# Kernel tuning notes

Hardware: AMD Instinct MI355X
Metric: run time of the kernel (lower is better)

## Reference

```python
import jax, jax.numpy as jnp
import numpy as np

B, S, D, H, INNER = 2, 2048, 1024, 16, 4096
HD = D // H
EPS = 1e-5


def setup_inputs() -> dict:
    key = jax.random.key(0)
    ks = jax.random.split(key, 8)

    def w(k, o, i):
        return jax.random.normal(k, (o, i), jnp.float32) * 0.02

    return {
        "hidden_states": jax.random.normal(ks[0], (B, S, D), jnp.float32),
        "attention_mask": jnp.ones((B, S), jnp.float32),
        "wq": w(ks[1], D, D), "bq": jnp.zeros((D,), jnp.float32),
        "wk": w(ks[2], D, D), "bk": jnp.zeros((D,), jnp.float32),
        "wv": w(ks[3], D, D), "bv": jnp.zeros((D,), jnp.float32),
        "wo": w(ks[4], D, D), "bo": jnp.zeros((D,), jnp.float32),
        "w1": w(ks[5], INNER, D), "b1": jnp.zeros((INNER,), jnp.float32),
        "w2": w(ks[6], D, INNER), "b2": jnp.zeros((D,), jnp.float32),
        "g1": jnp.ones((D,), jnp.float32), "be1": jnp.zeros((D,), jnp.float32),
        "g2": jnp.ones((D,), jnp.float32), "be2": jnp.zeros((D,), jnp.float32),
        "w_bits": 8,
        "a_bits": 8,
    }


def fake_quant(x, bits):
    # symmetric per-tensor fake quantization with straight-through estimator
    qmax = 2.0 ** (bits - 1) - 1.0
    scale = jnp.maximum(jnp.max(jnp.abs(x)), 1e-8) / qmax
    q = jnp.round(jnp.clip(x / scale, -qmax, qmax)) * scale
    return x + jax.lax.stop_gradient(q - x)


def qlinear(x, w, b, w_bits, a_bits):
    return fake_quant(x, a_bits) @ fake_quant(w, w_bits).T + b


def layernorm(x, g, b):
    m = jnp.mean(x, axis=-1, keepdims=True)
    v = jnp.mean((x - m) ** 2, axis=-1, keepdims=True)
    return (x - m) * jax.lax.rsqrt(v + EPS) * g + b


def reference(hidden_states, attention_mask, wq, bq, wk, bk, wv, bv, wo, bo,
              w1, b1, w2, b2, g1, be1, g2, be2, w_bits, a_bits):
    # --- attention sub-block ---
    residual = hidden_states
    x = layernorm(hidden_states, g1, be1)
    q = qlinear(x, wq, bq, w_bits, a_bits).reshape(B, S, H, HD)
    k = qlinear(x, wk, bk, w_bits, a_bits).reshape(B, S, H, HD)
    v = qlinear(x, wv, bv, w_bits, a_bits).reshape(B, S, H, HD)
    scores = jnp.einsum("bqhd,bkhd->bhqk", q, k) / jnp.sqrt(jnp.float32(HD))
    scores = scores + (1.0 - attention_mask)[:, None, None, :] * -10000.0
    probs = jax.nn.softmax(scores, axis=-1)
    attn = jnp.einsum("bhqk,bkhd->bqhd", probs, v).reshape(B, S, D)
    attn = qlinear(attn, wo, bo, w_bits, a_bits)
    hidden = residual + attn
    # --- MLP sub-block ---
    residual = hidden
    x = layernorm(hidden, g2, be2)
    x = qlinear(x, w1, b1, w_bits, a_bits)
    x = jax.nn.gelu(x, approximate=False)
    x = qlinear(x, w2, b2, w_bits, a_bits)
    return residual + x
```

## Files before the change

### kernel.cpp

```cpp
#include <hip/hip_runtime.h>
#include <hip/hip_bf16.h>
#include <math.h>

typedef __bf16 bf16;
typedef __bf16 bf16x8 __attribute__((ext_vector_type(8)));
typedef __bf16 bf16x4 __attribute__((ext_vector_type(4)));
typedef float  f32x4  __attribute__((ext_vector_type(4)));
typedef float  f32x16 __attribute__((ext_vector_type(16)));
typedef unsigned int u32x4 __attribute__((ext_vector_type(4)));

static constexpr int B_  = 2;
static constexpr int S_  = 2048;
static constexpr int D_  = 1024;
static constexpr int H_  = 16;
static constexpr int HD_ = 64;
static constexpr int I_  = 4096;
static constexpr int NT  = B_ * S_;

__device__ __forceinline__ void atomicMaxF(float* p, float v) {
  atomicMax((unsigned int*)p, __float_as_uint(v));
}

__device__ __forceinline__ f32x4 mfma16(bf16x8 a, bf16x8 b, f32x4 c) {
  return __builtin_amdgcn_mfma_f32_16x16x32_bf16(a, b, c, 0, 0, 0);
}

__device__ __forceinline__ f32x16 mfma32(bf16x8 a, bf16x8 b, f32x16 c) {
  return __builtin_amdgcn_mfma_f32_32x32x16_bf16(a, b, c, 0, 0, 0);
}

__device__ __forceinline__ void gload16(const void* g, void* lds) {
  __builtin_amdgcn_global_load_lds(
      (const __attribute__((address_space(1))) void*)g,
      (__attribute__((address_space(3))) void*)lds, 16, 0, 0);
}

__device__ __forceinline__ float quant1(float x, float scale, float qmax) {
  return rintf(fminf(fmaxf(x / scale, -qmax), qmax)) * scale;
}

__device__ __forceinline__ void stage64b(const bf16* __restrict__ g, int rs, bf16* lds, int t) {
  #pragma unroll
  for (int r = 0; r < 4; r++) {
    const int cl  = r * 128 + t;
    const int row = cl >> 3;
    const int scr = (cl & 7) ^ (row & 7);
    gload16(g + (size_t)row * rs + scr * 8,
            (char*)lds + (size_t)(r * 128 + (t & 64)) * 16);
  }
}

__global__ __launch_bounds__(256) void k_prep(const float* __restrict__ mask,
                                              float* __restrict__ madd, float* __restrict__ scal) {
  constexpr float MSK2 = -14426.950408889634f;
  const int i = blockIdx.x * 256 + threadIdx.x;
  if (blockIdx.x == 0 && threadIdx.x < 32) scal[threadIdx.x] = 0.f;
  if (i < B_ * S_) madd[i] = (1.0f - mask[i]) * MSK2;
}

struct WArgs {
  const float* w[6];
  bf16* q[6];
  size_t n4[6];
};

__global__ __launch_bounds__(256) void k_absmax6(WArgs a, float* __restrict__ slots) {
  const int z = blockIdx.z;
  const float* __restrict__ x = a.w[z];
  const size_t n4 = a.n4[z];
  size_t i = (size_t)blockIdx.x * 256 + threadIdx.x;
  const size_t stride = (size_t)gridDim.x * 256;
  float m = 0.f;
  for (; i < n4; i += stride) {
    float4 v = ((const float4*)x)[i];
    m = fmaxf(m, fmaxf(fmaxf(fabsf(v.x), fabsf(v.y)), fmaxf(fabsf(v.z), fabsf(v.w))));
  }
  #pragma unroll
  for (int o = 32; o; o >>= 1) m = fmaxf(m, __shfl_xor(m, o));
  __shared__ float red[4];
  if ((threadIdx.x & 63) == 0) red[threadIdx.x >> 6] = m;
  __syncthreads();
  if (threadIdx.x == 0)
    atomicMaxF(slots + z, fmaxf(fmaxf(red[0], red[1]), fmaxf(red[2], red[3])));
}

__global__ __launch_bounds__(256) void k_quant6(WArgs a, const float* __restrict__ slots,
                                                const int* __restrict__ bits) {
  const int z = blockIdx.z;
  const float* __restrict__ x = a.w[z];
  bf16* __restrict__ y = a.q[z];
  const size_t n4 = a.n4[z];
  const float qmax  = (float)((1 << (*bits - 1)) - 1);
  const float scale = fmaxf(slots[z], 1e-8f) / qmax;
  size_t i = (size_t)blockIdx.x * 256 + threadIdx.x;
  const size_t stride = (size_t)gridDim.x * 256;
  for (; i < n4; i += stride) {
    float4 v = ((const float4*)x)[i];
    bf16x4 o;
    o[0] = (bf16)quant1(v.x, scale, qmax);
    o[1] = (bf16)quant1(v.y, scale, qmax);
    o[2] = (bf16)quant1(v.z, scale, qmax);
    o[3] = (bf16)quant1(v.w, scale, qmax);
    ((bf16x4*)y)[i] = o;
  }
}

__global__ __launch_bounds__(256) void k_quant(const float* __restrict__ x, bf16* __restrict__ y,
                                               const float* __restrict__ slot,
                                               const int* __restrict__ bits, size_t n4) {
  const float qmax  = (float)((1 << (*bits - 1)) - 1);
  const float scale = fmaxf(*slot, 1e-8f) / qmax;
  size_t i = (size_t)blockIdx.x * 256 + threadIdx.x;
  const size_t stride = (size_t)gridDim.x * 256;
  for (; i < n4; i += stride) {
    float4 v = ((const float4*)x)[i];
    bf16x4 o;
    o[0] = (bf16)quant1(v.x, scale, qmax);
    o[1] = (bf16)quant1(v.y, scale, qmax);
    o[2] = (bf16)quant1(v.z, scale, qmax);
    o[3] = (bf16)quant1(v.w, scale, qmax);
    ((bf16x4*)y)[i] = o;
  }
}

__global__ __launch_bounds__(256) void k_quant_ip(bf16* __restrict__ x,
                                                  const float* __restrict__ slot,
                                                  const int* __restrict__ bits, size_t n8) {
  const float qmax  = (float)((1 << (*bits - 1)) - 1);
  const float scale = fmaxf(*slot, 1e-8f) / qmax;
  size_t i = (size_t)blockIdx.x * 256 + threadIdx.x;
  if (i >= n8) return;
  bf16x8 v = ((const bf16x8*)x)[i];
  #pragma unroll
  for (int j = 0; j < 8; j++) v[j] = (bf16)quant1((float)v[j], scale, qmax);
  ((bf16x8*)x)[i] = v;
}

__global__ __launch_bounds__(256) void k_ln(const float* __restrict__ x, const float* __restrict__ g,
                                            const float* __restrict__ be, float* __restrict__ y,
                                            float* __restrict__ slot) {
  const int row = blockIdx.x, t = threadIdx.x;
  const float4 v = ((const float4*)(x + (size_t)row * D_))[t];
  float s = v.x + v.y + v.z + v.w;
  float q = v.x * v.x + v.y * v.y + v.z * v.z + v.w * v.w;
  #pragma unroll
  for (int o = 32; o; o >>= 1) { s += __shfl_xor(s, o); q += __shfl_xor(q, o); }
  __shared__ float red[8];
  const int wid = t >> 6;
  if ((t & 63) == 0) { red[wid] = s; red[4 + wid] = q; }
  __syncthreads();
  s = red[0] + red[1] + red[2] + red[3];
  q = red[4] + red[5] + red[6] + red[7];
  const float mean = s * (1.f / D_);
  const float rstd = rsqrtf(q * (1.f / D_) - mean * mean + 1e-5f);
  const float4 gv = ((const float4*)g)[t];
  const float4 bv = ((const float4*)be)[t];
  float4 o;
  o.x = (v.x - mean) * rstd * gv.x + bv.x;
  o.y = (v.y - mean) * rstd * gv.y + bv.y;
  o.z = (v.z - mean) * rstd * gv.z + bv.z;
  o.w = (v.w - mean) * rstd * gv.w + bv.w;
  ((float4*)(y + (size_t)row * D_))[t] = o;
  float m = fmaxf(fmaxf(fabsf(o.x), fabsf(o.y)), fmaxf(fabsf(o.z), fabsf(o.w)));
  #pragma unroll
  for (int oo = 32; oo; oo >>= 1) m = fmaxf(m, __shfl_xor(m, oo));
  __syncthreads();
  if ((t & 63) == 0) red[wid] = m;
  __syncthreads();
  if (t == 0) atomicMaxF(slot, fmaxf(fmaxf(red[0], red[1]), fmaxf(red[2], red[3])));
}

struct GemmArgs {
  const bf16* A;
  const bf16* B0; const bf16* B1; const bf16* B2;
  const float* bias0; const float* bias1; const float* bias2;
  void* out0; void* out1; void* out2;
  const float* res;
  float* slot;
  int K; int ldc;
};

template <int MODE, int MT>
__global__ __launch_bounds__(256) void k_gemm(GemmArgs a) {
  constexpr int TM = MT * 32;
  __shared__ __align__(16) bf16 As[TM * 64];
  __shared__ __align__(16) bf16 Bs[128 * 64];
  const int t = threadIdx.x, wid = t >> 6, lane = t & 63;
  const int grp = lane >> 4, l15 = lane & 15;
  const int wm = wid >> 1, wn = wid & 1;
  const size_t m0 = (size_t)blockIdx.x * TM, n0 = (size_t)blockIdx.y * 128;
  const int K = a.K, ldc = a.ldc;

  const bf16* Bw; const float* bias; void* outv;
  if constexpr (MODE == 0) {
    const int z = blockIdx.z;
    Bw   = z == 0 ? a.B0 : (z == 1 ? a.B1 : a.B2);
    bias = z == 0 ? a.bias0 : (z == 1 ? a.bias1 : a.bias2);
    outv = z == 0 ? a.out0 : (z == 1 ? a.out1 : a.out2);
  } else {
    Bw = a.B0; bias = a.bias0; outv = a.out0;
  }

  const f32x4 zero = {0.f, 0.f, 0.f, 0.f};
  f32x4 acc[MT][4];
  #pragma unroll
  for (int m = 0; m < MT; m++)
    #pragma unroll
    for (int n = 0; n < 4; n++) acc[m][n] = zero;

  for (int kt = 0; kt < K; kt += 64) {
    #pragma unroll
    for (int r = 0; r < MT; r++) {
      const int cl = r * 256 + t;
      const int row = cl >> 3, c = cl & 7;
      gload16(a.A + (m0 + row) * (size_t)K + kt + ((c ^ (row & 7)) * 8),
              (char*)As + (size_t)(r * 256 + (t & 192)) * 16);
    }
    #pragma unroll
    for (int r = 0; r < 4; r++) {
      const int cl = r * 256 + t;
      const int row = cl >> 3, c = cl & 7;
      gload16(Bw + (n0 + row) * (size_t)K + kt + ((c ^ (row & 7)) * 8),
              (char*)Bs + (size_t)(r * 256 + (t & 192)) * 16);
    }
    __syncthreads();
    #pragma unroll
    for (int ks = 0; ks < 2; ks++) {
      bf16x8 bfv[4];
      #pragma unroll
      for (int n = 0; n < 4; n++) {
        const int rb = wn * 64 + n * 16 + l15;
        bfv[n] = *(const bf16x8*)(Bs + rb * 64 + (((ks * 4 + grp) ^ (rb & 7)) * 8));
      }
      #pragma unroll
      for (int m = 0; m < MT; m++) {
        const int ra = wm * (MT * 16) + m * 16 + l15;
        const bf16x8 af = *(const bf16x8*)(As + ra * 64 + (((ks * 4 + grp) ^ (ra & 7)) * 8));
        #pragma unroll
        for (int n = 0; n < 4; n++)
          acc[m][n] = mfma16(af, bfv[n], acc[m][n]);
      }
    }
    __syncthreads();
  }

  const size_t gr0 = m0 + wm * (MT * 16) + grp * 4;
  const size_t gc0 = n0 + wn * 64 + l15;

  if constexpr (MODE == 0) {
    if (blockIdx.z == 2) {
      #pragma unroll
      for (int n = 0; n < 4; n++) {
        const size_t gc = gc0 + n * 16;
        const float bc = bias[gc];
        #pragma unroll
        for (int m = 0; m < MT; m++) {
          const size_t gr = gr0 + m * 16;
          const size_t bb = gr >> 11, s0 = gr & (S_ - 1);
          bf16x4 vv;
          #pragma unroll
          for (int i = 0; i < 4; i++) vv[i] = (bf16)(acc[m][n][i] + bc);
          *(bf16x4*)((bf16*)outv + bb * (size_t)D_ * S_ + gc * S_ + s0) = vv;
        }
      }
      return;
    }
  }

  float lmax = 0.f;
  #pragma unroll
  for (int n = 0; n < 4; n++) {
    const size_t gc = gc0 + n * 16;
    const float bc = bias[gc];
    #pragma unroll
    for (int m = 0; m < MT; m++) {
      const size_t gr = gr0 + m * 16;
      #pragma unroll
      for (int i = 0; i < 4; i++) {
        const float v = acc[m][n][i] + bc;
        const size_t idx = (gr + i) * (size_t)ldc + gc;
        if constexpr (MODE == 0) {
          ((bf16*)outv)[idx] = (bf16)v;
        } else if constexpr (MODE == 1) {
          ((float*)outv)[idx] = v + a.res[idx];
        } else {
          const float gl = 0.5f * v * (1.0f + erff(v * 0.7071067811865475f));
          ((bf16*)outv)[idx] = (bf16)gl;
          lmax = fmaxf(lmax, fabsf(gl));
        }
      }
    }
  }
  if constexpr (MODE == 2) {
    #pragma unroll
    for (int o = 32; o; o >>= 1) lmax = fmaxf(lmax, __shfl_xor(lmax, o));
    __shared__ float red[4];
    if (lane == 0) red[wid] = lmax;
    __syncthreads();
    if (t == 0) atomicMaxF(a.slot, fmaxf(fmaxf(red[0], red[1]), fmaxf(red[2], red[3])));
  }
}

__global__ __launch_bounds__(128) void k_attn(const bf16* __restrict__ qb, const bf16* __restrict__ kb,
                                              const bf16* __restrict__ vt, const float* __restrict__ madd,
                                              float* __restrict__ out, float* __restrict__ slot) {
  constexpr float SCL2 = 0.18033688011112042f;
  constexpr float THR  = 8.0f;
  constexpr int NTILE  = S_ / 64;
  __shared__ __align__(16) bf16 Ks[2][64 * 64];
  __shared__ __align__(16) bf16 Vs[2][64 * 64];
  __shared__ float red[2];
  const int t = threadIdx.x, wid = t >> 6, lane = t & 63;
  const int l31 = lane & 31, hi = lane >> 5;
  const int b = blockIdx.y >> 4, h = blockIdx.y & 15;
  const size_t qkbase = ((size_t)b * S_) * D_ + (size_t)h * HD_;
  const size_t vtbase = (size_t)b * D_ * S_ + (size_t)h * HD_ * S_;
  const int q = blockIdx.x * 64 + wid * 32 + l31;

  bf16x8 qf[4];
  #pragma unroll
  for (int j = 0; j < 4; j++)
    qf[j] = *(const bf16x8*)(qb + qkbase + (size_t)q * D_ + j * 16 + hi * 8);

  f32x16 ao0, ao1;
  #pragma unroll
  for (int r = 0; r < 16; r++) { ao0[r] = 0.f; ao1[r] = 0.f; }
  float mi = -INFINITY, li = 0.f;
  unsigned pk[16];
  f32x4 mv[2][4];
  const float* mp = madd + (size_t)b * S_ + hi * 4;
  const int xk = (l31 & 7);

  auto qk_softmax = [&](const bf16* Kb) {
    f32x16 s0, s1;
    #pragma unroll
    for (int r = 0; r < 16; r++) { s0[r] = 0.f; s1[r] = 0.f; }
    #pragma unroll
    for (int j = 0; j < 4; j++) {
      const int ch = j * 2 + hi;
      const bf16x8 kf0 = *(const bf16x8*)(Kb + l31 * 64 + (ch ^ xk) * 8);
      const bf16x8 kf1 = *(const bf16x8*)(Kb + (32 + l31) * 64 + (ch ^ xk) * 8);
      s0 = mfma32(kf0, qf[j], s0);
      s1 = mfma32(kf1, qf[j], s1);
    }
    float pv_[32];
    #pragma unroll
    for (int r = 0; r < 16; r++) pv_[r]      = s0[r] * SCL2 + mv[0][r >> 2][r & 3];
    #pragma unroll
    for (int r = 0; r < 16; r++) pv_[16 + r] = s1[r] * SCL2 + mv[1][r >> 2][r & 3];
    float m16[16];
    #pragma unroll
    for (int r = 0; r < 16; r++) m16[r] = fmaxf(pv_[r], pv_[16 + r]);
    #pragma unroll
    for (int r = 0; r < 8; r++) m16[r] = fmaxf(m16[r], m16[8 + r]);
    #pragma unroll
    for (int r = 0; r < 4; r++) m16[r] = fmaxf(m16[r], m16[4 + r]);
    float mx = fmaxf(fmaxf(m16[0], m16[1]), fmaxf(m16[2], m16[3]));
    mx = fmaxf(mx, __shfl_xor(mx, 32));
    if (!__all(mx - mi <= THR)) {
      const float mnew = fmaxf(mi, mx);
      const float co = exp2f(mi - mnew);
      li *= co;
      #pragma unroll
      for (int r = 0; r < 16; r++) { ao0[r] *= co; ao1[r] *= co; }
      mi = mnew;
    }
    #pragma unroll
    for (int r = 0; r < 32; r++) pv_[r] = exp2f(pv_[r] - mi);
    float sm[16];
    #pragma unroll
    for (int r = 0; r < 16; r++) sm[r] = pv_[r] + pv_[16 + r];
    #pragma unroll
    for (int r = 0; r < 8; r++) sm[r] += sm[8 + r];
    #pragma unroll
    for (int r = 0; r < 4; r++) sm[r] += sm[4 + r];
    li += (sm[0] + sm[1]) + (sm[2] + sm[3]);
    #pragma unroll
    for (int tt = 0; tt < 8; tt++) {
      asm("v_cvt_pk_bf16_f32 %0, %1, %2" : "=v"(pk[tt])     : "v"(pv_[2 * tt]),      "v"(pv_[2 * tt + 1]));
      asm("v_cvt_pk_bf16_f32 %0, %1, %2" : "=v"(pk[8 + tt]) : "v"(pv_[16 + 2 * tt]), "v"(pv_[16 + 2 * tt + 1]));
    }
    #pragma unroll
    for (int g = 0; g < 4; g++) {
      asm volatile("v_permlane32_swap_b32 %0, %1" : "+v"(pk[4 * g]),     "+v"(pk[4 * g + 2]));
      asm volatile("v_permlane32_swap_b32 %0, %1" : "+v"(pk[4 * g + 1]), "+v"(pk[4 * g + 3]));
    }
  };

  auto pv_accum = [&](const bf16* Vb) {
    #pragma unroll
    for (int j = 0; j < 4; j++) {
      const u32x4 w = {pk[4 * j], pk[4 * j + 1], pk[4 * j + 2], pk[4 * j + 3]};
      const bf16x8 pf = __builtin_bit_cast(bf16x8, w);
      const int ch = j * 2 + hi;
      const bf16x8 vf0 = *(const bf16x8*)(Vb + l31 * 64 + (ch ^ xk) * 8);
      const bf16x8 vf1 = *(const bf16x8*)(Vb + (32 + l31) * 64 + (ch ^ xk) * 8);
      ao0 = mfma32(vf0, pf, ao0);
      ao1 = mfma32(vf1, pf, ao1);
    }
  };

  #pragma unroll
  for (int kb2 = 0; kb2 < 2; kb2++)
    #pragma unroll
    for (int g = 0; g < 4; g++) mv[kb2][g] = *(const f32x4*)(mp + kb2 * 32 + g * 8);
  __builtin_amdgcn_sched_barrier(0);
  stage64b(kb + qkbase, D_, Ks[0], t);
  stage64b(vt + vtbase, S_, Vs[0], t);
  stage64b(kb + qkbase + (size_t)64 * D_, D_, Ks[1], t);
  __syncthreads();
  qk_softmax(Ks[0]);
  __syncthreads();

  for (int i = 0; i < NTILE; i++) {
    const int cur = i & 1;
    const bool last = (i == NTILE - 1);
    if (!last) {
      const int kt1 = (i + 1) * 64;
      #pragma unroll
      for (int kb2 = 0; kb2 < 2; kb2++)
        #pragma unroll
        for (int g = 0; g < 4; g++) mv[kb2][g] = *(const f32x4*)(mp + kt1 + kb2 * 32 + g * 8);
      __builtin_amdgcn_sched_barrier(0);
      if (i + 2 < NTILE) stage64b(kb + qkbase + (size_t)(i + 2) * 64 * D_, D_, Ks[cur], t);
      stage64b(vt + vtbase + (i + 1) * 64, S_, Vs[cur ^ 1], t);
    }
    pv_accum(Vs[cur]);
    if (!last) {
      qk_softmax(Ks[cur ^ 1]);
      __syncthreads();
    }
  }

  li += __shfl_xor(li, 32);
  const float invl = 1.0f / li;
  float lmax = 0.f;
  float* orow = out + qkbase + (size_t)q * D_;
  #pragma unroll
  for (int db2 = 0; db2 < 2; db2++) {
    #pragma unroll
    for (int rg = 0; rg < 4; rg++) {
      float4 o;
      o.x = (db2 ? ao1[rg * 4 + 0] : ao0[rg * 4 + 0]) * invl;
      o.y = (db2 ? ao1[rg * 4 + 1] : ao0[rg * 4 + 1]) * invl;
      o.z = (db2 ? ao1[rg * 4 + 2] : ao0[rg * 4 + 2]) * invl;
      o.w = (db2 ? ao1[rg * 4 + 3] : ao0[rg * 4 + 3]) * invl;
      *(float4*)(orow + db2 * 32 + rg * 8 + hi * 4) = o;
      lmax = fmaxf(lmax, fmaxf(fmaxf(fabsf(o.x), fabsf(o.y)), fmaxf(fabsf(o.z), fabsf(o.w))));
    }
  }
  #pragma unroll
  for (int o = 32; o; o >>= 1) lmax = fmaxf(lmax, __shfl_xor(lmax, o));
  if (lane == 0) red[wid] = lmax;
  __syncthreads();
  if (t == 0) atomicMaxF(slot, fmaxf(red[0], red[1]));
}

extern "C" void kernel_launch(void* const* d_in, const int* in_sizes, int n_in,
                              void* d_out, int out_size, void* d_ws, size_t ws_size,
                              hipStream_t stream) {
  const float* hs   = (const float*)d_in[0];
  const float* mask = (const float*)d_in[1];
  const float* wq = (const float*)d_in[2];  const float* bq = (const float*)d_in[3];
  const float* wk = (const float*)d_in[4];  const float* bk = (const float*)d_in[5];
  const float* wv = (const float*)d_in[6];  const float* bv = (const float*)d_in[7];
  const float* wo = (const float*)d_in[8];  const float* bo = (const float*)d_in[9];
  const float* w1 = (const float*)d_in[10]; const float* b1 = (const float*)d_in[11];
  const float* w2 = (const float*)d_in[12]; const float* b2 = (const float*)d_in[13];
  const float* g1 = (const float*)d_in[14]; const float* be1 = (const float*)d_in[15];
  const float* g2 = (const float*)d_in[16]; const float* be2 = (const float*)d_in[17];
  const int* wbits = (const int*)d_in[18];
  const int* abits = (const int*)d_in[19];

  char* ws = (char*)d_ws;
  size_t off = 0;
  float* scal = (float*)ws;                      off += 256;
  float* maddg= (float*)(ws + off);              off += (size_t)NT * 4;
  float* fbuf = (float*)(ws + off);              off += (size_t)NT * D_ * 4;
  bf16*  qx   = (bf16*)(ws + off);               off += (size_t)NT * D_ * 2;
  bf16*  qb   = (bf16*)(ws + off);               off += (size_t)NT * D_ * 2;
  bf16*  kbuf = (bf16*)(ws + off);               off += (size_t)NT * D_ * 2;
  bf16*  vbuf = (bf16*)(ws + off);               off += (size_t)NT * D_ * 2;
  float* h2   = (float*)(ws + off);              off += (size_t)NT * D_ * 4;
  bf16*  h1   = (bf16*)(ws + off);               off += (size_t)NT * I_ * 2;
  bf16*  wqq  = (bf16*)(ws + off);               off += (size_t)D_ * D_ * 2;
  bf16*  wkq  = (bf16*)(ws + off);               off += (size_t)D_ * D_ * 2;
  bf16*  wvq  = (bf16*)(ws + off);               off += (size_t)D_ * D_ * 2;
  bf16*  woq  = (bf16*)(ws + off);               off += (size_t)D_ * D_ * 2;
  bf16*  w1q  = (bf16*)(ws + off);               off += (size_t)I_ * D_ * 2;
  bf16*  w2q  = (bf16*)(ws + off);               off += (size_t)D_ * I_ * 2;
  if (ws_size < off) return;

  k_prep<<<NT / 256, 256, 0, stream>>>(mask, maddg, scal);

  const size_t nDD4 = (size_t)D_ * D_ / 4, nDI4 = (size_t)D_ * I_ / 4;
  WArgs wa;
  wa.w[0] = wq; wa.w[1] = wk; wa.w[2] = wv; wa.w[3] = wo; wa.w[4] = w1; wa.w[5] = w2;
  wa.q[0] = wqq; wa.q[1] = wkq; wa.q[2] = wvq; wa.q[3] = woq; wa.q[4] = w1q; wa.q[5] = w2q;
  wa.n4[0] = nDD4; wa.n4[1] = nDD4; wa.n4[2] = nDD4; wa.n4[3] = nDD4;
  wa.n4[4] = nDI4; wa.n4[5] = nDI4;
  k_absmax6<<<dim3(1024, 1, 6), 256, 0, stream>>>(wa, scal + 4);
  k_quant6<<<dim3(1024, 1, 6), 256, 0, stream>>>(wa, scal + 4, wbits);

  const size_t nND4 = (size_t)NT * D_ / 4;

  k_ln<<<NT, 256, 0, stream>>>(hs, g1, be1, fbuf, scal + 0);
  k_quant<<<2048, 256, 0, stream>>>(fbuf, qx, scal + 0, abits, nND4);
  {
    GemmArgs ga{};
    ga.A = qx; ga.B0 = wqq; ga.B1 = wkq; ga.B2 = wvq;
    ga.bias0 = bq; ga.bias1 = bk; ga.bias2 = bv;
    ga.out0 = qb; ga.out1 = kbuf; ga.out2 = vbuf;
    ga.K = D_; ga.ldc = D_;
    k_gemm<0, 4><<<dim3(NT / 128, D_ / 128, 3), 256, 0, stream>>>(ga);
  }

  k_attn<<<dim3(S_ / 64, B_ * H_), 128, 0, stream>>>(qb, kbuf, vbuf, maddg, fbuf, scal + 1);
  k_quant<<<2048, 256, 0, stream>>>(fbuf, qx, scal + 1, abits, nND4);
  {
    GemmArgs ga{};
    ga.A = qx; ga.B0 = woq; ga.bias0 = bo; ga.out0 = h2; ga.res = hs;
    ga.K = D_; ga.ldc = D_;
    k_gemm<1, 2><<<dim3(NT / 64, D_ / 128), 256, 0, stream>>>(ga);
  }

  k_ln<<<NT, 256, 0, stream>>>(h2, g2, be2, fbuf, scal + 2);
  k_quant<<<2048, 256, 0, stream>>>(fbuf, qx, scal + 2, abits, nND4);
  {
    GemmArgs ga{};
    ga.A = qx; ga.B0 = w1q; ga.bias0 = b1; ga.out0 = h1; ga.slot = scal + 3;
    ga.K = D_; ga.ldc = I_;
    k_gemm<2, 4><<<dim3(NT / 128, I_ / 128), 256, 0, stream>>>(ga);
  }
  k_quant_ip<<<(NT * (size_t)I_ / 8 + 255) / 256, 256, 0, stream>>>(h1, scal + 3, abits,
                                                                    (size_t)NT * I_ / 8);
  {
    GemmArgs ga{};
    ga.A = h1; ga.B0 = w2q; ga.bias0 = b2; ga.out0 = d_out; ga.res = h2;
    ga.K = I_; ga.ldc = D_;
    k_gemm<1, 2><<<dim3(NT / 64, D_ / 128), 256, 0, stream>>>(ga);
  }
}
```

Baseline: 495.1 us.

## Double-buffer GEMM LDS tiles and add fast no-mask path in attention

The GEMM kernel now double-buffers its A/B LDS tiles so the next K-slice is loaded while MFMAs run on the current one. The attention kernel is restructured into a single loop with K/V double buffering, dropping the previous software-pipelined QK/PV overlap. It also gains a runtime branch that skips the mask loads and adds when a flag shows the mask is all ones, folding the scale into the exp2. The prep kernel computes that flag with a wave reduction plus atomic, and a separate init kernel zeroes the scalars. Double buffering doubles GEMM LDS use, which may lower occupancy, and the simpler attention loop may lose the earlier QK/PV overlap.

Measured after the change: 493.8 us. No clear change (-0.3%).

```diff
diff --git a/kernel.cpp b/kernel.cpp
--- a/kernel.cpp
+++ b/kernel.cpp
@@ -50,12 +50,22 @@
   }
 }
 
+__global__ void k_init(float* s) {
+  if (threadIdx.x < 32) s[threadIdx.x] = 0.f;
+}
+
 __global__ __launch_bounds__(256) void k_prep(const float* __restrict__ mask,
                                               float* __restrict__ madd, float* __restrict__ scal) {
   constexpr float MSK2 = -14426.950408889634f;
   const int i = blockIdx.x * 256 + threadIdx.x;
-  if (blockIdx.x == 0 && threadIdx.x < 32) scal[threadIdx.x] = 0.f;
-  if (i < B_ * S_) madd[i] = (1.0f - mask[i]) * MSK2;
+  if (i < B_ * S_) {
+    const float mv = (1.0f - mask[i]) * MSK2;
+    madd[i] = mv;
+    float nz = fabsf(mv);
+    #pragma unroll
+    for (int o = 32; o; o >>= 1) nz = fmaxf(nz, __shfl_xor(nz, o));
+    if ((threadIdx.x & 63) == 0 && nz > 0.f) atomicMaxF(scal + 10, nz);
+  }
 }
 
 struct WArgs {
@@ -183,8 +193,8 @@
 template <int MODE, int MT>
 __global__ __launch_bounds__(256) void k_gemm(GemmArgs a) {
   constexpr int TM = MT * 32;
-  __shared__ __align__(16) bf16 As[TM * 64];
-  __shared__ __align__(16) bf16 Bs[128 * 64];
+  __shared__ __align__(16) bf16 As[2][TM * 64];
+  __shared__ __align__(16) bf16 Bs[2][128 * 64];
   const int t = threadIdx.x, wid = t >> 6, lane = t & 63;
   const int grp = lane >> 4, l15 = lane & 15;
   const int wm = wid >> 1, wn = wid & 1;
@@ -208,40 +218,47 @@
     #pragma unroll
     for (int n = 0; n < 4; n++) acc[m][n] = zero;
 
-  for (int kt = 0; kt < K; kt += 64) {
+  auto stage = [&](int kt, int buf) {
     #pragma unroll
     for (int r = 0; r < MT; r++) {
       const int cl = r * 256 + t;
       const int row = cl >> 3, c = cl & 7;
       gload16(a.A + (m0 + row) * (size_t)K + kt + ((c ^ (row & 7)) * 8),
-              (char*)As + (size_t)(r * 256 + (t & 192)) * 16);
+              (char*)&As[buf][0] + (size_t)(r * 256 + (t & 192)) * 16);
     }
     #pragma unroll
     for (int r = 0; r < 4; r++) {
       const int cl = r * 256 + t;
       const int row = cl >> 3, c = cl & 7;
       gload16(Bw + (n0 + row) * (size_t)K + kt + ((c ^ (row & 7)) * 8),
-              (char*)Bs + (size_t)(r * 256 + (t & 192)) * 16);
-    }
-    __syncthreads();
+              (char*)&Bs[buf][0] + (size_t)(r * 256 + (t & 192)) * 16);
+    }
+  };
+
+  stage(0, 0);
+  __syncthreads();
+  int cur = 0;
+  for (int kt = 0; kt < K; kt += 64) {
+    if (kt + 64 < K) stage(kt + 64, cur ^ 1);
     #pragma unroll
     for (int ks = 0; ks < 2; ks++) {
       bf16x8 bfv[4];
       #pragma unroll
       for (int n = 0; n < 4; n++) {
         const int rb = wn * 64 + n * 16 + l15;
-        bfv[n] = *(const bf16x8*)(Bs + rb * 64 + (((ks * 4 + grp) ^ (rb & 7)) * 8));
+        bfv[n] = *(const bf16x8*)(&Bs[cur][0] + rb * 64 + (((ks * 4 + grp) ^ (rb & 7)) * 8));
       }
       #pragma unroll
       for (int m = 0; m < MT; m++) {
         const int ra = wm * (MT * 16) + m * 16 + l15;
-        const bf16x8 af = *(const bf16x8*)(As + ra * 64 + (((ks * 4 + grp) ^ (ra & 7)) * 8));
+        const bf16x8 af = *(const bf16x8*)(&As[cur][0] + ra * 64 + (((ks * 4 + grp) ^ (ra & 7)) * 8));
         #pragma unroll
         for (int n = 0; n < 4; n++)
           acc[m][n] = mfma16(af, bfv[n], acc[m][n]);
       }
     }
     __syncthreads();
+    cur ^= 1;
   }
 
   const size_t gr0 = m0 + wm * (MT * 16) + grp * 4;
@@ -294,7 +311,7 @@
   if constexpr (MODE == 2) {
     #pragma unroll
     for (int o = 32; o; o >>= 1) lmax = fmaxf(lmax, __shfl_xor(lmax, o));
-    __shared__ float red[4];
+    float* red = (float*)&As[0][0];
     if (lane == 0) red[wid] = lmax;
     __syncthreads();
     if (t == 0) atomicMaxF(a.slot, fmaxf(fmaxf(red[0], red[1]), fmaxf(red[2], red[3])));
@@ -303,9 +320,10 @@
 
 __global__ __launch_bounds__(128) void k_attn(const bf16* __restrict__ qb, const bf16* __restrict__ kb,
                                               const bf16* __restrict__ vt, const float* __restrict__ madd,
-                                              float* __restrict__ out, float* __restrict__ slot) {
+                                              float* __restrict__ out, float* __restrict__ scal) {
   constexpr float SCL2 = 0.18033688011112042f;
   constexpr float THR  = 8.0f;
+  constexpr float THRR = THR / SCL2;
   constexpr int NTILE  = S_ / 64;
   __shared__ __align__(16) bf16 Ks[2][64 * 64];
   __shared__ __align__(16) bf16 Vs[2][64 * 64];
@@ -316,6 +334,7 @@
   const size_t qkbase = ((size_t)b * S_) * D_ + (size_t)h * HD_;
   const size_t vtbase = (size_t)b * D_ * S_ + (size_t)h * HD_ * S_;
   const int q = blockIdx.x * 64 + wid * 32 + l31;
+  const bool nomask = (scal[10] == 0.0f);
 
   bf16x8 qf[4];
   #pragma unroll
@@ -326,28 +345,52 @@
   #pragma unroll
   for (int r = 0; r < 16; r++) { ao0[r] = 0.f; ao1[r] = 0.f; }
   float mi = -INFINITY, li = 0.f;
-  unsigned pk[16];
-  f32x4 mv[2][4];
   const float* mp = madd + (size_t)b * S_ + hi * 4;
   const int xk = (l31 & 7);
 
-  auto qk_softmax = [&](const bf16* Kb) {
+  stage64b(kb + qkbase, D_, Ks[0], t);
+  stage64b(vt + vtbase, S_, Vs[0], t);
+  __syncthreads();
+  int cur = 0;
+
+  for (int i = 0; i < NTILE; i++) {
+    f32x4 mv[2][4];
+    if (!nomask) {
+      #pragma unroll
+      for (int kb2 = 0; kb2 < 2; kb2++)
+        #pragma unroll
+        for (int g = 0; g < 4; g++)
+          mv[kb2][g] = *(const f32x4*)(mp + i * 64 + kb2 * 32 + g * 8);
+      __builtin_amdgcn_sched_barrier(0);
+    }
+    if (i + 1 < NTILE) {
+      stage64b(kb + qkbase + (size_t)(i + 1) * 64 * D_, D_, Ks[cur ^ 1], t);
+      stage64b(vt + vtbase + (i + 1) * 64, S_, Vs[cur ^ 1], t);
+    }
+
     f32x16 s0, s1;
     #pragma unroll
     for (int r = 0; r < 16; r++) { s0[r] = 0.f; s1[r] = 0.f; }
     #pragma unroll
     for (int j = 0; j < 4; j++) {
       const int ch = j * 2 + hi;
-      const bf16x8 kf0 = *(const bf16x8*)(Kb + l31 * 64 + (ch ^ xk) * 8);
-      const bf16x8 kf1 = *(const bf16x8*)(Kb + (32 + l31) * 64 + (ch ^ xk) * 8);
+      const bf16x8 kf0 = *(const bf16x8*)(&Ks[cur][0] + l31 * 64 + (ch ^ xk) * 8);
+      const bf16x8 kf1 = *(const bf16x8*)(&Ks[cur][0] + (32 + l31) * 64 + (ch ^ xk) * 8);
       s0 = mfma32(kf0, qf[j], s0);
       s1 = mfma32(kf1, qf[j], s1);
     }
+
     float pv_[32];
-    #pragma unroll
-    for (int r = 0; r < 16; r++) pv_[r]      = s0[r] * SCL2 + mv[0][r >> 2][r & 3];
-    #pragma unroll
-    for (int r = 0; r < 16; r++) pv_[16 + r] = s1[r] * SCL2 + mv[1][r >> 2][r & 3];
+    if (nomask) {
+      #pragma unroll
+      for (int r = 0; r < 16; r++) { pv_[r] = s0[r]; pv_[16 + r] = s1[r]; }
+    } else {
+      #pragma unroll
+      for (int r = 0; r < 16; r++) {
+        pv_[r]      = s0[r] * SCL2 + mv[0][r >> 2][r & 3];
+        pv_[16 + r] = s1[r] * SCL2 + mv[1][r >> 2][r & 3];
+      }
+    }
     float m16[16];
     #pragma unroll
     for (int r = 0; r < 16; r++) m16[r] = fmaxf(pv_[r], pv_[16 + r]);
@@ -357,16 +400,24 @@
     for (int r = 0; r < 4; r++) m16[r] = fmaxf(m16[r], m16[4 + r]);
     float mx = fmaxf(fmaxf(m16[0], m16[1]), fmaxf(m16[2], m16[3]));
     mx = fmaxf(mx, __shfl_xor(mx, 32));
-    if (!__all(mx - mi <= THR)) {
+
+    const float thr = nomask ? THRR : THR;
+    if (!__all(mx - mi <= thr)) {
       const float mnew = fmaxf(mi, mx);
-      const float co = exp2f(mi - mnew);
+      const float co = nomask ? exp2f((mi - mnew) * SCL2) : exp2f(mi - mnew);
       li *= co;
       #pragma unroll
       for (int r = 0; r < 16; r++) { ao0[r] *= co; ao1[r] *= co; }
       mi = mnew;
     }
-    #pragma unroll
-    for (int r = 0; r < 32; r++) pv_[r] = exp2f(pv_[r] - mi);
+    if (nomask) {
+      const float mo = -mi * SCL2;
+      #pragma unroll
+      for (int r = 0; r < 32; r++) pv_[r] = exp2f(fmaf(pv_[r], SCL2, mo));
+    } else {
+      #pragma unroll
+      for (int r = 0; r < 32; r++) pv_[r] = exp2f(pv_[r] - mi);
+    }
     float sm[16];
     #pragma unroll
     for (int r = 0; r < 16; r++) sm[r] = pv_[r] + pv_[16 + r];
@@ -375,6 +426,8 @@
     #pragma unroll
     for (int r = 0; r < 4; r++) sm[r] += sm[4 + r];
     li += (sm[0] + sm[1]) + (sm[2] + sm[3]);
+
+    unsigned pk[16];
     #pragma unroll
     for (int tt = 0; tt < 8; tt++) {
       asm("v_cvt_pk_bf16_f32 %0, %1, %2" : "=v"(pk[tt])     : "v"(pv_[2 * tt]),      "v"(pv_[2 * tt + 1]));
@@ -385,51 +438,19 @@
       asm volatile("v_permlane32_swap_b32 %0, %1" : "+v"(pk[4 * g]),     "+v"(pk[4 * g + 2]));
       asm volatile("v_permlane32_swap_b32 %0, %1" : "+v"(pk[4 * g + 1]), "+v"(pk[4 * g + 3]));
     }
-  };
-
-  auto pv_accum = [&](const bf16* Vb) {
+
     #pragma unroll
     for (int j = 0; j < 4; j++) {
       const u32x4 w = {pk[4 * j], pk[4 * j + 1], pk[4 * j + 2], pk[4 * j + 3]};
       const bf16x8 pf = __builtin_bit_cast(bf16x8, w);
       const int ch = j * 2 + hi;
-      const bf16x8 vf0 = *(const bf16x8*)(Vb + l31 * 64 + (ch ^ xk) * 8);
-      const bf16x8 vf1 = *(const bf16x8*)(Vb + (32 + l31) * 64 + (ch ^ xk) * 8);
+      const bf16x8 vf0 = *(const bf16x8*)(&Vs[cur][0] + l31 * 64 + (ch ^ xk) * 8);
+      const bf16x8 vf1 = *(const bf16x8*)(&Vs[cur][0] + (32 + l31) * 64 + (ch ^ xk) * 8);
       ao0 = mfma32(vf0, pf, ao0);
       ao1 = mfma32(vf1, pf, ao1);
     }
-  };
-
-  #pragma unroll
-  for (int kb2 = 0; kb2 < 2; kb2++)
-    #pragma unroll
-    for (int g = 0; g < 4; g++) mv[kb2][g] = *(const f32x4*)(mp + kb2 * 32 + g * 8);
-  __builtin_amdgcn_sched_barrier(0);
-  stage64b(kb + qkbase, D_, Ks[0], t);
-  stage64b(vt + vtbase, S_, Vs[0], t);
-  stage64b(kb + qkbase + (size_t)64 * D_, D_, Ks[1], t);
-  __syncthreads();
-  qk_softmax(Ks[0]);
-  __syncthreads();
-
-  for (int i = 0; i < NTILE; i++) {
-    const int cur = i & 1;
-    const bool last = (i == NTILE - 1);
-    if (!last) {
-      const int kt1 = (i + 1) * 64;
-      #pragma unroll
-      for (int kb2 = 0; kb2 < 2; kb2++)
-        #pragma unroll
-        for (int g = 0; g < 4; g++) mv[kb2][g] = *(const f32x4*)(mp + kt1 + kb2 * 32 + g * 8);
-      __builtin_amdgcn_sched_barrier(0);
-      if (i + 2 < NTILE) stage64b(kb + qkbase + (size_t)(i + 2) * 64 * D_, D_, Ks[cur], t);
-      stage64b(vt + vtbase + (i + 1) * 64, S_, Vs[cur ^ 1], t);
-    }
-    pv_accum(Vs[cur]);
-    if (!last) {
-      qk_softmax(Ks[cur ^ 1]);
-      __syncthreads();
-    }
+    __syncthreads();
+    cur ^= 1;
   }
 
   li += __shfl_xor(li, 32);
@@ -453,7 +474,7 @@
   for (int o = 32; o; o >>= 1) lmax = fmaxf(lmax, __shfl_xor(lmax, o));
   if (lane == 0) red[wid] = lmax;
   __syncthreads();
-  if (t == 0) atomicMaxF(slot, fmaxf(red[0], red[1]));
+  if (t == 0) atomicMaxF(scal + 1, fmaxf(red[0], red[1]));
 }
 
 extern "C" void kernel_launch(void* const* d_in, const int* in_sizes, int n_in,
@@ -491,6 +512,7 @@
   bf16*  w2q  = (bf16*)(ws + off);               off += (size_t)D_ * I_ * 2;
   if (ws_size < off) return;
 
+  k_init<<<1, 64, 0, stream>>>(scal);
   k_prep<<<NT / 256, 256, 0, stream>>>(mask, maddg, scal);
 
   const size_t nDD4 = (size_t)D_ * D_ / 4, nDI4 = (size_t)D_ * I_ / 4;
@@ -515,7 +537,7 @@
     k_gemm<0, 4><<<dim3(NT / 128, D_ / 128, 3), 256, 0, stream>>>(ga);
   }
 
-  k_attn<<<dim3(S_ / 64, B_ * H_), 128, 0, stream>>>(qb, kbuf, vbuf, maddg, fbuf, scal + 1);
+  k_attn<<<dim3(S_ / 64, B_ * H_), 128, 0, stream>>>(qb, kbuf, vbuf, maddg, fbuf, scal);
   k_quant<<<2048, 256, 0, stream>>>(fbuf, qx, scal + 1, abits, nND4);
   {
     GemmArgs ga{};
```
